# Kernel optimization log

Measured on AMD Instinct MI355X. Metric: run time of the kernel, lower is better.

The kernel has to match this reference:

```python
import jax, jax.numpy as jnp
import numpy as np

HEADS = 16
KEY_SIZE = 64
SIZE_PER_HEAD = 64
OUT_DIM = HEADS * SIZE_PER_HEAD  # 1024
BIG = 1e10
B, LQ, LK = 2, 2048, 2048


def setup_inputs() -> dict:
    key = jax.random.key(0)
    ks = jax.random.split(key, 8)
    q = jax.random.normal(ks[0], (B, LQ, OUT_DIM), dtype=jnp.float32)
    k = jax.random.normal(ks[1], (B, LK, OUT_DIM), dtype=jnp.float32)
    v = jax.random.normal(ks[2], (B, LK, OUT_DIM), dtype=jnp.float32)
    v_mask = (jax.random.uniform(ks[3], (B, LK)) > 0.1).astype(jnp.float32)
    q_mask = (jax.random.uniform(ks[4], (B, LQ)) > 0.1).astype(jnp.float32)
    # bias-free Linear weights, torch layout [out_features, in_features]
    s = 1.0 / np.sqrt(OUT_DIM)
    Wq = jax.random.normal(ks[5], (HEADS * KEY_SIZE, OUT_DIM), dtype=jnp.float32) * s
    Wk = jax.random.normal(ks[6], (HEADS * KEY_SIZE, OUT_DIM), dtype=jnp.float32) * s
    Wv = jax.random.normal(ks[7], (OUT_DIM, OUT_DIM), dtype=jnp.float32) * s
    return {"q": q, "k": k, "v": v, "v_mask": v_mask, "q_mask": q_mask,
            "Wq": Wq, "Wk": Wk, "Wv": Wv}


def _attention(q, k, v, v_mask, q_mask, Wq, Wk, Wv):
    b, lq, _ = q.shape
    lk = k.shape[1]
    # projections (torch Linear: x @ W.T)
    qw = jnp.einsum('bld,ed->ble', q, Wq).reshape(b, lq, HEADS, KEY_SIZE)
    kw = jnp.einsum('bld,ed->ble', k, Wk).reshape(b, lk, HEADS, KEY_SIZE)
    vw = jnp.einsum('bld,ed->ble', v, Wv).reshape(b, lk, HEADS, SIZE_PER_HEAD)
    # scores [B, H, Lq, Lk]
    a = jnp.einsum('bqhd,bkhd->bhqk', qw, kw) / np.sqrt(KEY_SIZE).astype(np.float32)
    # additive key-padding mask: a - (1 - v_mask) * BIG, broadcast over H and Lq
    a = a - (1.0 - v_mask)[:, None, None, :] * BIG
    # mask_right=True branch: mask = (1 - triu(ones, diag=1)) * BIG, i.e. lower
    # triangle INCLUDING the diagonal is penalized (faithful to source quirk).
    causal = jnp.tril(jnp.ones((lq, lk), dtype=a.dtype)) * BIG  # [Lq, Lk]
    a = a - causal[None, None, :, :]
    a = jax.nn.softmax(a, axis=-1)
    # output [B, Lq, H*dv]
    o = jnp.einsum('bhqk,bkhd->bqhd', a, vw).reshape(b, lq, OUT_DIM)
    o = o * q_mask[:, :, None]
    return o


def reference(q, k, v, v_mask, q_mask, Wq, Wk, Wv):
    return _attention(q, k, v, v_mask, q_mask, Wq, Wk, Wv)
```

## Files before the change

### kernel.cpp

```cpp
#include <hip/hip_runtime.h>
#include <hip/hip_bf16.h>
#include <stdint.h>

#define B_    2
#define SEQ   2048
#define EMB   1024
#define BIGF  1e10f
#define LOG2E 1.4426950408889634f
#define BIG2F (1e10f * LOG2E)
#define C2    (0.125f * LOG2E)

typedef unsigned short u16;
typedef __attribute__((ext_vector_type(4))) u16      u16x4;
typedef __attribute__((ext_vector_type(8))) short    bf8;
typedef __attribute__((ext_vector_type(4))) float    f4;
typedef __attribute__((ext_vector_type(4))) float    fv4;

__device__ inline float bf2f(u16 u){ union{uint32_t i; float f;} v; v.i = ((uint32_t)u) << 16; return v.f; }
__device__ inline u16 f2bf(float f){ union{float f; uint32_t i;} v; v.f = f;
                                     uint32_t r = v.i + 0x7fffu + ((v.i >> 16) & 1u); return (u16)(r >> 16); }
__device__ inline float exp2_hw(float x){ float r; asm("v_exp_f32 %0, %1" : "=v"(r) : "v"(x)); return r; }

__device__ inline void gl_lds16(const void* g, void* l){
  __builtin_amdgcn_global_load_lds((const __attribute__((address_space(1))) uint32_t*)g,
                                   (__attribute__((address_space(3))) uint32_t*)l, 16, 0, 0);
}

struct CvtArgs { const float* src[6]; u16* dst[6]; int n[6]; };

__global__ __launch_bounds__(256) void cvt_bf16(CvtArgs a)
{
  const int seg = blockIdx.y;
  const float* __restrict__ s = a.src[seg];
  u16* __restrict__ d = a.dst[seg];
  const int n = a.n[seg];
  const int i = (blockIdx.x * 256 + threadIdx.x) * 8;
  if (i >= n) return;
  fv4 x0 = *(const fv4*)(s + i);
  fv4 x1 = *(const fv4*)(s + i + 4);
  union { bf8 v; u16 u[8]; } o;
#pragma unroll
  for (int j = 0; j < 4; j++) { o.u[j] = f2bf(x0[j]); o.u[4 + j] = f2bf(x1[j]); }
  *(bf8*)(d + i) = o.v;
}

__global__ __launch_bounds__(256) void proj_gemm(
    const u16* __restrict__ Xq, const u16* __restrict__ Xk, const u16* __restrict__ Xv,
    const u16* __restrict__ Wq, const u16* __restrict__ Wk, const u16* __restrict__ Wv,
    u16* __restrict__ QH, u16* __restrict__ KH, u16* __restrict__ VTB)
{
  __shared__ u16 smem[18432];
  const int z = blockIdx.z;
  const u16* X = (z == 0) ? Xq : ((z == 1) ? Xk : Xv);
  const u16* W = (z == 0) ? Wq : ((z == 1) ? Wk : Wv);

  const int tid  = threadIdx.x;
  const int lane = tid & 63;
  const int w    = tid >> 6;
  const int wm   = w >> 1, wn = w & 1;
  const int m0   = blockIdx.x * 128;
  const int n0   = blockIdx.y * 128;
  const int col  = lane & 15, quad = lane >> 4;
  const int sq8  = (quad ^ ((col >> 1) & 3)) * 8;

  const int srow = w * 16 + (lane >> 2);
  const int sc   = ((lane & 3) ^ ((lane >> 3) & 3)) * 8;
  const size_t gA0 = (size_t)(m0 + srow) * 1024 + sc;
  const size_t gA1 = (size_t)(m0 + 64 + srow) * 1024 + sc;
  const size_t gB0 = (size_t)(n0 + srow) * 1024 + sc;
  const size_t gB1 = (size_t)(n0 + 64 + srow) * 1024 + sc;
  const int ldst = w * 512 + lane * 8;

  const f4 zero = {0.f, 0.f, 0.f, 0.f};
  f4 acc[4][4];
#pragma unroll
  for (int i = 0; i < 4; i++)
#pragma unroll
    for (int j = 0; j < 4; j++) acc[i][j] = zero;

  {
    gl_lds16(X + gA0, &smem[ldst]);
    gl_lds16(X + gA1, &smem[2048 + ldst]);
    gl_lds16(W + gB0, &smem[4096 + ldst]);
    gl_lds16(W + gB1, &smem[6144 + ldst]);
  }

#pragma unroll 2
  for (int t = 0; t < 32; t++) {
    __syncthreads();
    if (t + 1 < 32) {
      const int kn = (t + 1) * 32;
      u16* nb = smem + ((t + 1) & 1) * 8192;
      gl_lds16(X + gA0 + kn, &nb[ldst]);
      gl_lds16(X + gA1 + kn, &nb[2048 + ldst]);
      gl_lds16(W + gB0 + kn, &nb[4096 + ldst]);
      gl_lds16(W + gB1 + kn, &nb[6144 + ldst]);
    }
    const u16* cA = smem + (t & 1) * 8192;
    const u16* cB = cA + 4096;
    bf8 a[4], b[4];
#pragma unroll
    for (int tt = 0; tt < 4; tt++) a[tt] = *(const bf8*)&cA[(wm * 64 + tt * 16 + col) * 32 + sq8];
#pragma unroll
    for (int tt = 0; tt < 4; tt++) b[tt] = *(const bf8*)&cB[(wn * 64 + tt * 16 + col) * 32 + sq8];
#pragma unroll
    for (int mt = 0; mt < 4; mt++)
#pragma unroll
      for (int nt = 0; nt < 4; nt++)
        acc[mt][nt] = __builtin_amdgcn_mfma_f32_16x16x32_bf16(a[mt], b[nt], acc[mt][nt], 0, 0, 0);
  }

  __syncthreads();
  u16* ep = &smem[w * 4608];

  if (z == 2) {
#pragma unroll
    for (int mt = 0; mt < 4; mt++)
#pragma unroll
      for (int nt = 0; nt < 4; nt++) {
        u16x4 pk = { f2bf(acc[mt][nt][0]), f2bf(acc[mt][nt][1]),
                     f2bf(acc[mt][nt][2]), f2bf(acc[mt][nt][3]) };
        *(u16x4*)&ep[(nt * 16 + col) * 72 + mt * 16 + quad * 4] = pk;
      }
  } else {
#pragma unroll
    for (int mt = 0; mt < 4; mt++)
#pragma unroll
      for (int nt = 0; nt < 4; nt++)
#pragma unroll
        for (int r = 0; r < 4; r++)
          ep[(mt * 16 + quad * 4 + r) * 72 + nt * 16 + col] = f2bf(acc[mt][nt][r]);
  }

  const int bb = m0 >> 11;
  const int h  = (n0 >> 6) + wn;
  const int bh = bb * 16 + h;

  if (z == 0) {
    const int qbase = (m0 & 2047) + wm * 64;
    u16* dst = QH + ((size_t)bh * SEQ + qbase) * 64;
#pragma unroll
    for (int i = 0; i < 8; i++) {
      const int f  = i * 1024 + lane * 16;
      const int ml = i * 8 + (lane >> 3), nl = (lane & 7) * 8;
      *(bf8*)(dst + (f >> 1)) = *(const bf8*)&ep[ml * 72 + nl];
    }
  } else if (z == 1) {
    const int kt = (((m0 & 2047) >> 6) + wm);
    u16* dst = KH + (((size_t)bh * 32 + kt) << 12);
#pragma unroll
    for (int i = 0; i < 8; i++) {
      const int f   = i * 1024 + lane * 16;
      const int dh  = f >> 12;
      const int klc = (f >> 6) & 63;
      const int dlo = (lane & 3) * 8;
      const int fs  = f ^ (((klc >> 1) & 3) << 4);
      *(bf8*)(dst + (fs >> 1)) = *(const bf8*)&ep[klc * 72 + dh * 32 + dlo];
    }
  } else {
    const int kt = (((m0 & 2047) >> 6) + wm);
    u16* dst = VTB + (((size_t)bh * 32 + kt) << 12);
#pragma unroll
    for (int i = 0; i < 8; i++) {
      const int f   = i * 1024 + lane * 16;
      const int kk  = f >> 12;
      const int d   = (f >> 6) & 63;
      const int klo = (lane & 3) * 8;
      const int fs  = f ^ (((d >> 1) & 3) << 4);
      *(bf8*)(dst + (fs >> 1)) = *(const bf8*)&ep[d * 72 + kk * 32 + klo];
    }
  }
}

__global__ __launch_bounds__(256) void sumv(const u16* __restrict__ VTB,
                                            const float* __restrict__ vmask,
                                            float* __restrict__ fb)
{
  const int w = threadIdx.x >> 6, lane = threadIdx.x & 63;
  const int gw = blockIdx.x * 4 + w;
  const int b = gw >> 10, e = gw & 1023;
  const int h = e >> 6, d = e & 63;
  const int bh = b * 16 + h;
  const float* vm = vmask + b * SEQ;
  const int ksw = (lane & 31) ^ (((d >> 1) & 3) << 3);
  float s = 0.f, c = 0.f;
  for (int kt = 0; kt < 32; kt++) {
    const u16 val = VTB[(((size_t)bh * 32 + kt) << 12) + (lane >> 5) * 2048 + d * 32 + ksw];
    const float m = vm[kt * 64 + lane];
    s += m * bf2f(val); c += m;
  }
#pragma unroll
  for (int o = 1; o < 64; o <<= 1) { s += __shfl_xor(s, o); c += __shfl_xor(c, o); }
  if (lane == 0) fb[gw] = s / c;
}

__global__ __launch_bounds__(256) void attn(
    const u16* __restrict__ QH, const u16* __restrict__ KH, const u16* __restrict__ VTB,
    const float* __restrict__ vmask, const float* __restrict__ qmask,
    const float* __restrict__ fb, float* __restrict__ OUT)
{
  __shared__ float pen[SEQ];
  __shared__ u16   sK[2][4096];
  __shared__ u16   sV[2][4096];
  __shared__ u16   P[4 * 16 * 72];

  const int tid = threadIdx.x, lane = tid & 63, w = tid >> 6;
  const int i   = blockIdx.x;
  const int xcd = i & 7;
  const int j   = i >> 3;
  const int qx  = j >> 2;
  const int bh  = xcd + 8 * (j & 3);
  const int b = bh >> 4, h = bh & 15;
  const int col = lane & 15, quad = lane >> 4;
  const int sq8 = (quad ^ ((col >> 1) & 3)) * 8;
  const int wb = w * 16 * 72;

  for (int t = tid; t < SEQ; t += 256)
    pen[t] = (1.0f - vmask[b * SEQ + t]) * BIG2F;

  const u16* kbase = KH  + (((size_t)bh * 32) << 12);
  const u16* vbase = VTB + (((size_t)bh * 32) << 12);

  const int q0 = qx * 64;

  bf8 bQ[2];
#pragma unroll
  for (int dh = 0; dh < 2; dh++)
    bQ[dh] = *(const bf8*)&QH[((size_t)bh * SEQ + q0 + w * 16 + col) * 64 + dh * 32 + quad * 8];

  const f4 zero = {0.f, 0.f, 0.f, 0.f};
  f4 accO[4];
  float l_acc = 0.f;
#pragma unroll
  for (int t = 0; t < 4; t++) accO[t] = zero;

  {
    const size_t toff = ((size_t)qx << 12) + w * 1024 + lane * 8;
    gl_lds16(kbase + toff,       &sK[0][w * 1024]);
    gl_lds16(kbase + toff + 512, &sK[0][w * 1024 + 512]);
    gl_lds16(vbase + toff,       &sV[0][w * 1024]);
    gl_lds16(vbase + toff + 512, &sV[0][w * 1024 + 512]);
  }

  const int ntile = 32 - qx;
  for (int it = 0; it < ntile; it++) {
    __syncthreads();
    if (it + 1 < ntile) {
      const int nb = (it + 1) & 1;
      const size_t toff = ((size_t)(qx + it + 1) << 12) + w * 1024 + lane * 8;
      gl_lds16(kbase + toff,       &sK[nb][w * 1024]);
      gl_lds16(kbase + toff + 512, &sK[nb][w * 1024 + 512]);
      gl_lds16(vbase + toff,       &sV[nb][w * 1024]);
      gl_lds16(vbase + toff + 512, &sV[nb][w * 1024 + 512]);
    }
    const u16* cK = sK[it & 1];
    const u16* cV = sV[it & 1];
    const int k0 = (qx + it) * 64;

    f4 accS[4];
#pragma unroll
    for (int t = 0; t < 4; t++) accS[t] = zero;
    __builtin_amdgcn_s_setprio(1);
#pragma unroll
    for (int nt = 0; nt < 4; nt++)
#pragma unroll
      for (int dh = 0; dh < 2; dh++) {
        bf8 aK = *(const bf8*)&cK[dh * 2048 + (nt * 16 + col) * 32 + sq8];
        accS[nt] = __builtin_amdgcn_mfma_f32_16x16x32_bf16(aK, bQ[dh], accS[nt], 0, 0, 0);
      }
    __builtin_amdgcn_s_setprio(0);

    float p[4][4];
    fv4 pv[4];
#pragma unroll
    for (int nt = 0; nt < 4; nt++) pv[nt] = *(const fv4*)&pen[k0 + nt * 16 + quad * 4];
    if (it == 0) {
#pragma unroll
      for (int nt = 0; nt < 4; nt++)
#pragma unroll
        for (int r = 0; r < 4; r++) {
          float sv = fmaf(accS[nt][r], C2, -pv[nt][r]);
          if (nt * 16 + quad * 4 + r <= w * 16 + col) sv -= BIG2F;
          p[nt][r] = exp2_hw(sv);
        }
    } else {
#pragma unroll
      for (int nt = 0; nt < 4; nt++)
#pragma unroll
        for (int r = 0; r < 4; r++)
          p[nt][r] = exp2_hw(fmaf(accS[nt][r], C2, -pv[nt][r]));
    }
#pragma unroll
    for (int nt = 0; nt < 4; nt++)
      l_acc += (p[nt][0] + p[nt][1]) + (p[nt][2] + p[nt][3]);

#pragma unroll
    for (int nt = 0; nt < 4; nt++) {
      union { u16x4 v; u16 u[4]; } pk;
      union { __hip_bfloat162 h2; u16 u[2]; } c0, c1;
      float2 f01; f01.x = p[nt][0]; f01.y = p[nt][1];
      float2 f23; f23.x = p[nt][2]; f23.y = p[nt][3];
      c0.h2 = __float22bfloat162_rn(f01);
      c1.h2 = __float22bfloat162_rn(f23);
      pk.u[0] = c0.u[0]; pk.u[1] = c0.u[1]; pk.u[2] = c1.u[0]; pk.u[3] = c1.u[1];
      *(u16x4*)&P[wb + col * 72 + nt * 16 + quad * 4] = pk.v;
    }

    __builtin_amdgcn_s_setprio(1);
#pragma unroll
    for (int kk = 0; kk < 2; kk++) {
      bf8 bP = *(const bf8*)&P[wb + col * 72 + kk * 32 + quad * 8];
#pragma unroll
      for (int nt = 0; nt < 4; nt++) {
        bf8 aV = *(const bf8*)&cV[kk * 2048 + (nt * 16 + col) * 32 + sq8];
        accO[nt] = __builtin_amdgcn_mfma_f32_16x16x32_bf16(aV, bP, accO[nt], 0, 0, 0);
      }
    }
    __builtin_amdgcn_s_setprio(0);
  }

  float l = l_acc;
  l += __shfl_xor(l, 16); l += __shfl_xor(l, 32);
  const int q = q0 + w * 16 + col;
  const float qm = qmask[b * SEQ + q];
  float* op = OUT + (size_t)(b * SEQ + q) * EMB + h * 64;
  if (l == 0.0f) {
#pragma unroll
    for (int nt = 0; nt < 4; nt++) {
      fv4 f = *(const fv4*)&fb[b * 1024 + h * 64 + nt * 16 + quad * 4];
      f *= qm;
      *(fv4*)(op + nt * 16 + quad * 4) = f;
    }
  } else {
    const float s = qm / l;
#pragma unroll
    for (int nt = 0; nt < 4; nt++) {
      fv4 f = { accO[nt][0] * s, accO[nt][1] * s, accO[nt][2] * s, accO[nt][3] * s };
      *(fv4*)(op + nt * 16 + quad * 4) = f;
    }
  }
}

extern "C" void kernel_launch(void* const* d_in, const int* in_sizes, int n_in,
                              void* d_out, int out_size, void* d_ws, size_t ws_size,
                              hipStream_t stream)
{
  const float* q  = (const float*)d_in[0];
  const float* k  = (const float*)d_in[1];
  const float* v  = (const float*)d_in[2];
  const float* vm = (const float*)d_in[3];
  const float* qm = (const float*)d_in[4];
  const float* Wq = (const float*)d_in[5];
  const float* Wk = (const float*)d_in[6];
  const float* Wv = (const float*)d_in[7];
  float* out = (float*)d_out;

  const size_t NBIG = (size_t)B_ * SEQ * EMB;
  const size_t NW   = (size_t)EMB * EMB;

  u16* qb  = (u16*)d_ws;
  u16* kb  = qb  + NBIG;
  u16* vb  = kb  + NBIG;
  u16* Wqb = vb  + NBIG;
  u16* Wkb = Wqb + NW;
  u16* Wvb = Wkb + NW;
  u16* QH  = Wvb + NW;
  u16* KH  = QH  + NBIG;
  u16* VTB = KH  + NBIG;
  float* fb = (float*)(VTB + NBIG);

  CvtArgs ca;
  ca.src[0] = q;  ca.dst[0] = qb;  ca.n[0] = (int)NBIG;
  ca.src[1] = k;  ca.dst[1] = kb;  ca.n[1] = (int)NBIG;
  ca.src[2] = v;  ca.dst[2] = vb;  ca.n[2] = (int)NBIG;
  ca.src[3] = Wq; ca.dst[3] = Wqb; ca.n[3] = (int)NW;
  ca.src[4] = Wk; ca.dst[4] = Wkb; ca.n[4] = (int)NW;
  ca.src[5] = Wv; ca.dst[5] = Wvb; ca.n[5] = (int)NW;

  cvt_bf16<<<dim3((unsigned)(NBIG / 8 / 256), 6, 1), 256, 0, stream>>>(ca);
  proj_gemm<<<dim3(32, 8, 3), 256, 0, stream>>>(qb, kb, vb, Wqb, Wkb, Wvb, QH, KH, VTB);
  sumv<<<dim3(512, 1, 1), 256, 0, stream>>>(VTB, vm, fb);
  attn<<<dim3(1024, 1, 1), 256, 0, stream>>>(QH, KH, VTB, vm, qm, fb, out);
}
```

Measured before the change: 187.7 us.

## Deepen projection GEMM prefetch to two stages in flight with explicit waitcnts

```diff
diff --git a/kernel.cpp b/kernel.cpp
--- a/kernel.cpp
+++ b/kernel.cpp
@@ -71,6 +71,13 @@
   const size_t gB1 = (size_t)(n0 + 64 + srow) * 1024 + sc;
   const int ldst = w * 512 + lane * 8;
 
+#define PSTAGE(nb, kn) do { \
+    gl_lds16(X + gA0 + (kn), &(nb)[ldst]); \
+    gl_lds16(X + gA1 + (kn), &(nb)[2048 + ldst]); \
+    gl_lds16(W + gB0 + (kn), &(nb)[4096 + ldst]); \
+    gl_lds16(W + gB1 + (kn), &(nb)[6144 + ldst]); \
+  } while (0)
+
   const f4 zero = {0.f, 0.f, 0.f, 0.f};
   f4 acc[4][4];
 #pragma unroll
@@ -78,24 +85,14 @@
 #pragma unroll
     for (int j = 0; j < 4; j++) acc[i][j] = zero;
 
-  {
-    gl_lds16(X + gA0, &smem[ldst]);
-    gl_lds16(X + gA1, &smem[2048 + ldst]);
-    gl_lds16(W + gB0, &smem[4096 + ldst]);
-    gl_lds16(W + gB1, &smem[6144 + ldst]);
-  }
+  PSTAGE(smem, 0);
+  PSTAGE((smem + 8192), 32);
 
 #pragma unroll 2
-  for (int t = 0; t < 32; t++) {
-    __syncthreads();
-    if (t + 1 < 32) {
-      const int kn = (t + 1) * 32;
-      u16* nb = smem + ((t + 1) & 1) * 8192;
-      gl_lds16(X + gA0 + kn, &nb[ldst]);
-      gl_lds16(X + gA1 + kn, &nb[2048 + ldst]);
-      gl_lds16(W + gB0 + kn, &nb[4096 + ldst]);
-      gl_lds16(W + gB1 + kn, &nb[6144 + ldst]);
-    }
+  for (int t = 0; t < 31; t++) {
+    asm volatile("s_waitcnt vmcnt(4)" ::: "memory");
+    __builtin_amdgcn_s_barrier();
+    __builtin_amdgcn_sched_barrier(0);
     const u16* cA = smem + (t & 1) * 8192;
     const u16* cB = cA + 4096;
     bf8 a[4], b[4];
@@ -103,12 +100,41 @@
     for (int tt = 0; tt < 4; tt++) a[tt] = *(const bf8*)&cA[(wm * 64 + tt * 16 + col) * 32 + sq8];
 #pragma unroll
     for (int tt = 0; tt < 4; tt++) b[tt] = *(const bf8*)&cB[(wn * 64 + tt * 16 + col) * 32 + sq8];
+    asm volatile("s_waitcnt lgkmcnt(0)" ::: "memory");
+    __builtin_amdgcn_sched_barrier(0);
+    __builtin_amdgcn_s_barrier();
+    if (t < 30) {
+      u16* nb = smem + (t & 1) * 8192;
+      PSTAGE(nb, (t + 2) * 32);
+    }
+    __builtin_amdgcn_s_setprio(1);
 #pragma unroll
     for (int mt = 0; mt < 4; mt++)
 #pragma unroll
       for (int nt = 0; nt < 4; nt++)
         acc[mt][nt] = __builtin_amdgcn_mfma_f32_16x16x32_bf16(a[mt], b[nt], acc[mt][nt], 0, 0, 0);
-  }
+    __builtin_amdgcn_s_setprio(0);
+  }
+  {
+    asm volatile("s_waitcnt vmcnt(0)" ::: "memory");
+    __builtin_amdgcn_s_barrier();
+    __builtin_amdgcn_sched_barrier(0);
+    const u16* cA = smem + 8192;
+    const u16* cB = cA + 4096;
+    bf8 a[4], b[4];
+#pragma unroll
+    for (int tt = 0; tt < 4; tt++) a[tt] = *(const bf8*)&cA[(wm * 64 + tt * 16 + col) * 32 + sq8];
+#pragma unroll
+    for (int tt = 0; tt < 4; tt++) b[tt] = *(const bf8*)&cB[(wn * 64 + tt * 16 + col) * 32 + sq8];
+    __builtin_amdgcn_s_setprio(1);
+#pragma unroll
+    for (int mt = 0; mt < 4; mt++)
+#pragma unroll
+      for (int nt = 0; nt < 4; nt++)
+        acc[mt][nt] = __builtin_amdgcn_mfma_f32_16x16x32_bf16(a[mt], b[nt], acc[mt][nt], 0, 0, 0);
+    __builtin_amdgcn_s_setprio(0);
+  }
+#undef PSTAGE
 
   __syncthreads();
   u16* ep = &smem[w * 4608];
```

Result: faster. 178.7 us (-4.8%).

## Fuse fp32-to-bf16 activation conversion into projection GEMM and deepen attention prefetch

Applied to the files above, without the earlier changes.

```diff
diff --git a/kernel.cpp b/kernel.cpp
--- a/kernel.cpp
+++ b/kernel.cpp
@@ -26,7 +26,18 @@
                                    (__attribute__((address_space(3))) uint32_t*)l, 16, 0, 0);
 }
 
-struct CvtArgs { const float* src[6]; u16* dst[6]; int n[6]; };
+__device__ inline bf8 pack8(fv4 a, fv4 b){
+  union { bf8 v; u16 u[8]; } o;
+  union { __hip_bfloat162 h2; u16 u[2]; } c;
+  float2 t;
+  t.x = a[0]; t.y = a[1]; c.h2 = __float22bfloat162_rn(t); o.u[0] = c.u[0]; o.u[1] = c.u[1];
+  t.x = a[2]; t.y = a[3]; c.h2 = __float22bfloat162_rn(t); o.u[2] = c.u[0]; o.u[3] = c.u[1];
+  t.x = b[0]; t.y = b[1]; c.h2 = __float22bfloat162_rn(t); o.u[4] = c.u[0]; o.u[5] = c.u[1];
+  t.x = b[2]; t.y = b[3]; c.h2 = __float22bfloat162_rn(t); o.u[6] = c.u[0]; o.u[7] = c.u[1];
+  return o.v;
+}
+
+struct CvtArgs { const float* src[3]; u16* dst[3]; int n[3]; };
 
 __global__ __launch_bounds__(256) void cvt_bf16(CvtArgs a)
 {
@@ -38,21 +49,18 @@
   if (i >= n) return;
   fv4 x0 = *(const fv4*)(s + i);
   fv4 x1 = *(const fv4*)(s + i + 4);
-  union { bf8 v; u16 u[8]; } o;
-#pragma unroll
-  for (int j = 0; j < 4; j++) { o.u[j] = f2bf(x0[j]); o.u[4 + j] = f2bf(x1[j]); }
-  *(bf8*)(d + i) = o.v;
+  *(bf8*)(d + i) = pack8(x0, x1);
 }
 
 __global__ __launch_bounds__(256) void proj_gemm(
-    const u16* __restrict__ Xq, const u16* __restrict__ Xk, const u16* __restrict__ Xv,
+    const float* __restrict__ Xq, const float* __restrict__ Xk, const float* __restrict__ Xv,
     const u16* __restrict__ Wq, const u16* __restrict__ Wk, const u16* __restrict__ Wv,
     u16* __restrict__ QH, u16* __restrict__ KH, u16* __restrict__ VTB)
 {
   __shared__ u16 smem[18432];
   const int z = blockIdx.z;
-  const u16* X = (z == 0) ? Xq : ((z == 1) ? Xk : Xv);
-  const u16* W = (z == 0) ? Wq : ((z == 1) ? Wk : Wv);
+  const float* X = (z == 0) ? Xq : ((z == 1) ? Xk : Xv);
+  const u16*   W = (z == 0) ? Wq : ((z == 1) ? Wk : Wv);
 
   const int tid  = threadIdx.x;
   const int lane = tid & 63;
@@ -63,10 +71,15 @@
   const int col  = lane & 15, quad = lane >> 4;
   const int sq8  = (quad ^ ((col >> 1) & 3)) * 8;
 
+  const int r    = tid >> 1;
+  const int c0   = (tid & 1) * 2;
+  const int s_   = (r >> 1) & 3;
+  const size_t gAf = (size_t)(m0 + r) * 1024 + (tid & 1) * 16;
+  const int wA0  = (r * 4 + (c0 ^ s_)) * 8;
+  const int wA1  = (r * 4 + ((c0 + 1) ^ s_)) * 8;
+
   const int srow = w * 16 + (lane >> 2);
   const int sc   = ((lane & 3) ^ ((lane >> 3) & 3)) * 8;
-  const size_t gA0 = (size_t)(m0 + srow) * 1024 + sc;
-  const size_t gA1 = (size_t)(m0 + 64 + srow) * 1024 + sc;
   const size_t gB0 = (size_t)(n0 + srow) * 1024 + sc;
   const size_t gB1 = (size_t)(n0 + 64 + srow) * 1024 + sc;
   const int ldst = w * 512 + lane * 8;
@@ -79,35 +92,55 @@
     for (int j = 0; j < 4; j++) acc[i][j] = zero;
 
   {
-    gl_lds16(X + gA0, &smem[ldst]);
-    gl_lds16(X + gA1, &smem[2048 + ldst]);
+    const float* g = X + gAf;
+    fv4 x0 = *(const fv4*)g, x1 = *(const fv4*)(g + 4);
+    fv4 x2 = *(const fv4*)(g + 8), x3 = *(const fv4*)(g + 12);
+    *(bf8*)&smem[wA0] = pack8(x0, x1);
+    *(bf8*)&smem[wA1] = pack8(x2, x3);
     gl_lds16(W + gB0, &smem[4096 + ldst]);
     gl_lds16(W + gB1, &smem[6144 + ldst]);
   }
+  asm volatile("s_waitcnt vmcnt(0) lgkmcnt(0)" ::: "memory");
+  __builtin_amdgcn_sched_barrier(0);
+  __builtin_amdgcn_s_barrier();
 
 #pragma unroll 2
   for (int t = 0; t < 32; t++) {
-    __syncthreads();
-    if (t + 1 < 32) {
-      const int kn = (t + 1) * 32;
-      u16* nb = smem + ((t + 1) & 1) * 8192;
-      gl_lds16(X + gA0 + kn, &nb[ldst]);
-      gl_lds16(X + gA1 + kn, &nb[2048 + ldst]);
-      gl_lds16(W + gB0 + kn, &nb[4096 + ldst]);
-      gl_lds16(W + gB1 + kn, &nb[6144 + ldst]);
-    }
     const u16* cA = smem + (t & 1) * 8192;
     const u16* cB = cA + 4096;
+    u16* nA = smem + ((t + 1) & 1) * 8192;
+    u16* nB = nA + 4096;
+
     bf8 a[4], b[4];
 #pragma unroll
     for (int tt = 0; tt < 4; tt++) a[tt] = *(const bf8*)&cA[(wm * 64 + tt * 16 + col) * 32 + sq8];
 #pragma unroll
     for (int tt = 0; tt < 4; tt++) b[tt] = *(const bf8*)&cB[(wn * 64 + tt * 16 + col) * 32 + sq8];
+
+    fv4 x0, x1, x2, x3;
+    if (t + 1 < 32) {
+      const float* g = X + gAf + (t + 1) * 32;
+      x0 = *(const fv4*)g;       x1 = *(const fv4*)(g + 4);
+      x2 = *(const fv4*)(g + 8); x3 = *(const fv4*)(g + 12);
+      gl_lds16(W + gB0 + (t + 1) * 32, &nB[ldst]);
+      gl_lds16(W + gB1 + (t + 1) * 32, &nB[2048 + ldst]);
+    }
+
+    __builtin_amdgcn_s_setprio(1);
 #pragma unroll
     for (int mt = 0; mt < 4; mt++)
 #pragma unroll
       for (int nt = 0; nt < 4; nt++)
         acc[mt][nt] = __builtin_amdgcn_mfma_f32_16x16x32_bf16(a[mt], b[nt], acc[mt][nt], 0, 0, 0);
+    __builtin_amdgcn_s_setprio(0);
+
+    if (t + 1 < 32) {
+      *(bf8*)&nA[wA0] = pack8(x0, x1);
+      *(bf8*)&nA[wA1] = pack8(x2, x3);
+    }
+    asm volatile("s_waitcnt vmcnt(0) lgkmcnt(0)" ::: "memory");
+    __builtin_amdgcn_sched_barrier(0);
+    __builtin_amdgcn_s_barrier();
   }
 
   __syncthreads();
@@ -128,8 +161,8 @@
 #pragma unroll
       for (int nt = 0; nt < 4; nt++)
 #pragma unroll
-        for (int r = 0; r < 4; r++)
-          ep[(mt * 16 + quad * 4 + r) * 72 + nt * 16 + col] = f2bf(acc[mt][nt][r]);
+        for (int rr = 0; rr < 4; rr++)
+          ep[(mt * 16 + quad * 4 + rr) * 72 + nt * 16 + col] = f2bf(acc[mt][nt][rr]);
   }
 
   const int bb = m0 >> 11;
@@ -234,28 +267,31 @@
 #pragma unroll
   for (int t = 0; t < 4; t++) accO[t] = zero;
 
-  {
-    const size_t toff = ((size_t)qx << 12) + w * 1024 + lane * 8;
-    gl_lds16(kbase + toff,       &sK[0][w * 1024]);
-    gl_lds16(kbase + toff + 512, &sK[0][w * 1024 + 512]);
-    gl_lds16(vbase + toff,       &sV[0][w * 1024]);
-    gl_lds16(vbase + toff + 512, &sV[0][w * 1024 + 512]);
-  }
+#define ASTAGE(BUF, KT) do { \
+    const size_t toff_ = ((size_t)(KT) << 12) + w * 1024 + lane * 8; \
+    gl_lds16(kbase + toff_,       &sK[(BUF)][w * 1024]); \
+    gl_lds16(kbase + toff_ + 512, &sK[(BUF)][w * 1024 + 512]); \
+    gl_lds16(vbase + toff_,       &sV[(BUF)][w * 1024]); \
+    gl_lds16(vbase + toff_ + 512, &sV[(BUF)][w * 1024 + 512]); \
+  } while (0)
 
   const int ntile = 32 - qx;
+  ASTAGE(0, qx);
+  ASTAGE(1, qx + 1);
+
   for (int it = 0; it < ntile; it++) {
-    __syncthreads();
-    if (it + 1 < ntile) {
-      const int nb = (it + 1) & 1;
-      const size_t toff = ((size_t)(qx + it + 1) << 12) + w * 1024 + lane * 8;
-      gl_lds16(kbase + toff,       &sK[nb][w * 1024]);
-      gl_lds16(kbase + toff + 512, &sK[nb][w * 1024 + 512]);
-      gl_lds16(vbase + toff,       &sV[nb][w * 1024]);
-      gl_lds16(vbase + toff + 512, &sV[nb][w * 1024 + 512]);
-    }
+    if (it + 1 < ntile) asm volatile("s_waitcnt vmcnt(4) lgkmcnt(0)" ::: "memory");
+    else                asm volatile("s_waitcnt vmcnt(0) lgkmcnt(0)" ::: "memory");
+    __builtin_amdgcn_s_barrier();
+    __builtin_amdgcn_sched_barrier(0);
+
     const u16* cK = sK[it & 1];
     const u16* cV = sV[it & 1];
     const int k0 = (qx + it) * 64;
+
+    fv4 pv[4];
+#pragma unroll
+    for (int nt = 0; nt < 4; nt++) pv[nt] = *(const fv4*)&pen[k0 + nt * 16 + quad * 4];
 
     f4 accS[4];
 #pragma unroll
@@ -271,9 +307,6 @@
     __builtin_amdgcn_s_setprio(0);
 
     float p[4][4];
-    fv4 pv[4];
-#pragma unroll
-    for (int nt = 0; nt < 4; nt++) pv[nt] = *(const fv4*)&pen[k0 + nt * 16 + quad * 4];
     if (it == 0) {
 #pragma unroll
       for (int nt = 0; nt < 4; nt++)
@@ -297,12 +330,12 @@
 #pragma unroll
     for (int nt = 0; nt < 4; nt++) {
       union { u16x4 v; u16 u[4]; } pk;
-      union { __hip_bfloat162 h2; u16 u[2]; } c0, c1;
+      union { __hip_bfloat162 h2; u16 u[2]; } cc0, cc1;
       float2 f01; f01.x = p[nt][0]; f01.y = p[nt][1];
       float2 f23; f23.x = p[nt][2]; f23.y = p[nt][3];
-      c0.h2 = __float22bfloat162_rn(f01);
-      c1.h2 = __float22bfloat162_rn(f23);
-      pk.u[0] = c0.u[0]; pk.u[1] = c0.u[1]; pk.u[2] = c1.u[0]; pk.u[3] = c1.u[1];
+      cc0.h2 = __float22bfloat162_rn(f01);
+      cc1.h2 = __float22bfloat162_rn(f23);
+      pk.u[0] = cc0.u[0]; pk.u[1] = cc0.u[1]; pk.u[2] = cc1.u[0]; pk.u[3] = cc1.u[1];
       *(u16x4*)&P[wb + col * 72 + nt * 16 + quad * 4] = pk.v;
     }
 
@@ -317,7 +350,13 @@
       }
     }
     __builtin_amdgcn_s_setprio(0);
-  }
+
+    asm volatile("s_waitcnt lgkmcnt(0)" ::: "memory");
+    __builtin_amdgcn_sched_barrier(0);
+    __builtin_amdgcn_s_barrier();
+    if (it + 2 < ntile) { ASTAGE((it & 1), qx + it + 2); }
+  }
+#undef ASTAGE
 
   float l = l_acc;
   l += __shfl_xor(l, 16); l += __shfl_xor(l, 32);
@@ -358,10 +397,7 @@
   const size_t NBIG = (size_t)B_ * SEQ * EMB;
   const size_t NW   = (size_t)EMB * EMB;
 
-  u16* qb  = (u16*)d_ws;
-  u16* kb  = qb  + NBIG;
-  u16* vb  = kb  + NBIG;
-  u16* Wqb = vb  + NBIG;
+  u16* Wqb = (u16*)d_ws;
   u16* Wkb = Wqb + NW;
   u16* Wvb = Wkb + NW;
   u16* QH  = Wvb + NW;
@@ -370,15 +406,12 @@
   float* fb = (float*)(VTB + NBIG);
 
   CvtArgs ca;
-  ca.src[0] = q;  ca.dst[0] = qb;  ca.n[0] = (int)NBIG;
-  ca.src[1] = k;  ca.dst[1] = kb;  ca.n[1] = (int)NBIG;
-  ca.src[2] = v;  ca.dst[2] = vb;  ca.n[2] = (int)NBIG;
-  ca.src[3] = Wq; ca.dst[3] = Wqb; ca.n[3] = (int)NW;
-  ca.src[4] = Wk; ca.dst[4] = Wkb; ca.n[4] = (int)NW;
-  ca.src[5] = Wv; ca.dst[5] = Wvb; ca.n[5] = (int)NW;
-
-  cvt_bf16<<<dim3((unsigned)(NBIG / 8 / 256), 6, 1), 256, 0, stream>>>(ca);
-  proj_gemm<<<dim3(32, 8, 3), 256, 0, stream>>>(qb, kb, vb, Wqb, Wkb, Wvb, QH, KH, VTB);
+  ca.src[0] = Wq; ca.dst[0] = Wqb; ca.n[0] = (int)NW;
+  ca.src[1] = Wk; ca.dst[1] = Wkb; ca.n[1] = (int)NW;
+  ca.src[2] = Wv; ca.dst[2] = Wvb; ca.n[2] = (int)NW;
+
+  cvt_bf16<<<dim3((unsigned)(NW / 8 / 256), 3, 1), 256, 0, stream>>>(ca);
+  proj_gemm<<<dim3(32, 8, 3), 256, 0, stream>>>(q, k, v, Wqb, Wkb, Wvb, QH, KH, VTB);
   sumv<<<dim3(512, 1, 1), 256, 0, stream>>>(VTB, vm, fb);
   attn<<<dim3(1024, 1, 1), 256, 0, stream>>>(QH, KH, VTB, vm, qm, fb, out);
 }
```

New measurement: 209.6 us. +11.7%, slower.
